# Optimization experiments

Measured on AMD Instinct MI355X. Metric: run time of the kernel, lower is better.

The kernel has to match this reference:

```python
import jax, jax.numpy as jnp
import numpy as np

B, L, ENC, D, H, HD, MLP, R = 4, 512, 512, 1024, 16, 64, 4096, 32
NUM_BUCKETS, MAX_DISTANCE = 32, 128
EPS = 1e-6
NEG = -1e10


def rmsnorm(x, scale):
    var = jnp.mean(jnp.square(x), axis=-1, keepdims=True)
    return x * jax.lax.rsqrt(var + EPS) * scale


def rel_pos_bias(table, qlen, klen):
    # T5 causal (bidirectional=False) relative position bucketing.
    ctx = jnp.arange(qlen)[:, None]
    mem = jnp.arange(klen)[None, :]
    rp = mem - ctx                      # [q, k]
    n = -jnp.minimum(rp, 0)             # distance into the past
    max_exact = NUM_BUCKETS // 2
    is_small = n < max_exact
    large = max_exact + (
        jnp.log(jnp.maximum(n, 1).astype(jnp.float32) / max_exact)
        / np.log(MAX_DISTANCE / max_exact) * (NUM_BUCKETS - max_exact)
    ).astype(jnp.int32)
    large = jnp.minimum(large, NUM_BUCKETS - 1)
    bucket = jnp.where(is_small, n, large)
    return table[bucket].transpose(2, 0, 1)[None]  # [1, h, q, k]


def lora_dense(x, W, a, b):
    # x:[B,L,d]  W:[d,e]  a:[B,d,r]  b:[B,r,e]  -> xW + (xa)b per example
    out = jnp.einsum('bld,de->ble', x, W)
    low = jnp.einsum('bld,bdr->blr', x, a)
    return out + jnp.einsum('blr,bre->ble', low, b)


def attention(xq, xkv, Wq, Wk, Wv, Wo, qa, qb, ka, kb, va, vb, oa, ob, bias):
    b, ql, _ = xq.shape
    kl = xkv.shape[1]
    q = lora_dense(xq, Wq, qa, qb).reshape(b, ql, H, HD) * (1.0 / np.sqrt(HD))
    k = lora_dense(xkv, Wk, ka, kb).reshape(b, kl, H, HD)
    v = lora_dense(xkv, Wv, va, vb).reshape(b, kl, H, HD)
    scores = jnp.einsum('bqhd,bkhd->bhqk', q, k)
    if bias is not None:
        scores = scores + bias
    probs = jax.nn.softmax(scores, axis=-1)
    ctx = jnp.einsum('bhqk,bkhd->bqhd', probs, v).reshape(b, ql, H * HD)
    return lora_dense(ctx, Wo, oa, ob)


def setup_inputs() -> dict:
    key = jax.random.key(0)
    ks = jax.random.split(key, 32)
    s = 0.02
    inp = {
        'inputs':  jax.random.normal(ks[0], (B, L, D), jnp.float32),
        'encoded': jax.random.normal(ks[1], (B, ENC, D), jnp.float32),
        'lora_qa': jax.random.normal(ks[2], (B, 2, D, R), jnp.float32) * s,
        'lora_qb': jax.random.normal(ks[3], (B, 2, R, D), jnp.float32) * s,
        'lora_ka': jax.random.normal(ks[4], (B, 2, D, R), jnp.float32) * s,
        'lora_kb': jax.random.normal(ks[5], (B, 2, R, D), jnp.float32) * s,
        'lora_va': jax.random.normal(ks[6], (B, 2, D, R), jnp.float32) * s,
        'lora_vb': jax.random.normal(ks[7], (B, 2, R, D), jnp.float32) * s,
        'lora_oa': jax.random.normal(ks[8], (B, 2, D, R), jnp.float32) * s,
        'lora_ob': jax.random.normal(ks[9], (B, 2, R, D), jnp.float32) * s,
        'rel_table': jax.random.normal(ks[10], (NUM_BUCKETS, H), jnp.float32) * s,
        'ln1': jnp.ones((D,), jnp.float32),
        'ln2': jnp.ones((D,), jnp.float32),
        'ln3': jnp.ones((D,), jnp.float32),
        'sWq': jax.random.normal(ks[11], (D, H * HD), jnp.float32) * s,
        'sWk': jax.random.normal(ks[12], (D, H * HD), jnp.float32) * s,
        'sWv': jax.random.normal(ks[13], (D, H * HD), jnp.float32) * s,
        'sWo': jax.random.normal(ks[14], (H * HD, D), jnp.float32) * s,
        'cWq': jax.random.normal(ks[15], (D, H * HD), jnp.float32) * s,
        'cWk': jax.random.normal(ks[16], (D, H * HD), jnp.float32) * s,
        'cWv': jax.random.normal(ks[17], (D, H * HD), jnp.float32) * s,
        'cWo': jax.random.normal(ks[18], (H * HD, D), jnp.float32) * s,
        'wi0': jax.random.normal(ks[19], (D, MLP), jnp.float32) * s,
        'wi1': jax.random.normal(ks[20], (D, MLP), jnp.float32) * s,
        'wo_mlp': jax.random.normal(ks[21], (MLP, D), jnp.float32) * s,
    }
    return inp


def reference(inputs, encoded, lora_qa, lora_qb, lora_ka, lora_kb, lora_va, lora_vb,
              lora_oa, lora_ob, rel_table, ln1, ln2, ln3,
              sWq, sWk, sWv, sWo, cWq, cWk, cWv, cWo, wi0, wi1, wo_mlp):
    l = inputs.shape[1]
    causal = jnp.tril(jnp.ones((l, l), dtype=bool))
    dec_bias = rel_pos_bias(rel_table, l, l) + jnp.where(causal, 0.0, NEG)[None, None]

    # --- self-attention block ---
    x = rmsnorm(inputs, ln1)
    x = attention(x, x, sWq, sWk, sWv, sWo,
                  lora_qa[:, 0], lora_qb[:, 0], lora_ka[:, 0], lora_kb[:, 0],
                  lora_va[:, 0], lora_vb[:, 0], lora_oa[:, 0], lora_ob[:, 0],
                  dec_bias)
    x = x + inputs

    # --- cross-attention block ---
    y = rmsnorm(x, ln2)
    y = attention(y, encoded, cWq, cWk, cWv, cWo,
                  lora_qa[:, 1], lora_qb[:, 1], lora_ka[:, 1], lora_kb[:, 1],
                  lora_va[:, 1], lora_vb[:, 1], lora_oa[:, 1], lora_ob[:, 1],
                  None)
    y = y + x

    # --- gated-gelu MLP block (T5 v1.1 style) ---
    lz = rmsnorm(y, ln3)
    h = jax.nn.gelu(lz @ wi0, approximate=False) * (lz @ wi1)
    z = h @ wo_mlp + y
    return z
```

## Files before the change

kernel.cpp:

```cpp
#include <hip/hip_runtime.h>
#include <math.h>


#define DEV __device__ __forceinline__

typedef __bf16 bf16x8 __attribute__((ext_vector_type(8)));
typedef float floatx4 __attribute__((ext_vector_type(4)));

typedef __attribute__((address_space(1))) void* gas_ptr;
typedef __attribute__((address_space(3))) void* las_ptr;

DEV unsigned short f2bf(float f) {
  union { float f; unsigned int u; } v; v.f = f;
  unsigned int r = v.u + 0x7fffu + ((v.u >> 16) & 1u);
  return (unsigned short)(r >> 16);
}
DEV float bf2f(unsigned short u) {
  union { unsigned int u; float f; } v; v.u = ((unsigned int)u) << 16;
  return v.f;
}

#define GLOAD_LDS16(g, l) __builtin_amdgcn_global_load_lds((gas_ptr)(g), (las_ptr)(l), 16, 0, 0)

template<int NW>
DEV void stage_tile_sw(const char* gbase, char* lds, int nrows, int ldbytes, int wave, int lane) {
  int nchunks = nrows >> 3;
  int colb = (((lane & 7) ^ ((lane >> 3) & 7)) << 4);
  for (int c = wave; c < nchunks; c += NW) {
    int row = (c << 3) + (lane >> 3);
    GLOAD_LDS16(gbase + (size_t)row * ldbytes + colb, lds + (c << 10));
  }
}

template<int NW>
DEV void stage_tile256_sw(const char* gbase, char* lds, int nrows, int ldbytes, int wave, int lane) {
  int nchunks = nrows >> 2;
  for (int c = wave; c < nchunks; c += NW) {
    int row = (c << 2) + (lane >> 4);
    int key = row & 7;
    int colb = ((lane & 15) ^ key) << 4;
    GLOAD_LDS16(gbase + (size_t)row * ldbytes + colb, lds + (c << 10));
  }
}

template<int WM, int WN>
DEV void gemm_core(const unsigned short* A, const unsigned short* Bt, float* C,
                   int K, int lda, int ldb, int ldc, int m0, int n0,
                   char* ldsA, char* ldsB) {
  constexpr int NW = WM * WN;
  const int tid  = threadIdx.x;
  const int lane = tid & 63;
  const int wave = tid >> 6;
  const int wm   = wave % WM;
  const int wn   = wave / WM;
  const int quad = lane >> 4;
  const int l15  = lane & 15;
  const int key  = l15 & 7;

  floatx4 acc[4][4];
#pragma unroll
  for (int i = 0; i < 4; ++i)
#pragma unroll
    for (int j = 0; j < 4; ++j) acc[i][j] = (floatx4){0.f, 0.f, 0.f, 0.f};

  const char* gA = (const char*)(A + (size_t)m0 * lda);
  const char* gB = (const char*)(Bt + (size_t)n0 * ldb);

  for (int k0 = 0; k0 < K; k0 += 64) {
    stage_tile_sw<NW>(gA + (size_t)k0 * 2, ldsA, WM * 64, lda * 2, wave, lane);
    stage_tile_sw<NW>(gB + (size_t)k0 * 2, ldsB, WN * 64, ldb * 2, wave, lane);
    __syncthreads();
#pragma unroll
    for (int kk = 0; kk < 64; kk += 32) {
      bf16x8 af[4], bv[4];
      int off = (((kk >> 3) + quad) ^ key) << 4;
      const char* baseA = ldsA + (size_t)(wm * 64 + l15) * 128 + off;
      const char* baseB = ldsB + (size_t)(wn * 64 + l15) * 128 + off;
#pragma unroll
      for (int mi = 0; mi < 4; ++mi) af[mi] = *(const bf16x8*)(baseA + mi * 2048);
#pragma unroll
      for (int ni = 0; ni < 4; ++ni) bv[ni] = *(const bf16x8*)(baseB + ni * 2048);
#pragma unroll
      for (int mi = 0; mi < 4; ++mi)
#pragma unroll
        for (int ni = 0; ni < 4; ++ni)
          acc[mi][ni] = __builtin_amdgcn_mfma_f32_16x16x32_bf16(af[mi], bv[ni], acc[mi][ni], 0, 0, 0);
    }
    __syncthreads();
  }

#pragma unroll
  for (int mi = 0; mi < 4; ++mi) {
#pragma unroll
    for (int r = 0; r < 4; ++r) {
      int row = m0 + wm * 64 + mi * 16 + quad * 4 + r;
#pragma unroll
      for (int ni = 0; ni < 4; ++ni) {
        int col = n0 + wn * 64 + ni * 16 + l15;
        C[(size_t)row * ldc + col] = acc[mi][ni][r];
      }
    }
  }
}

__global__ __launch_bounds__(256) void k_gemm1s(const unsigned short* A, const unsigned short* Bt,
                                                float* Cpart, size_t pstride,
                                                int Kchunk, int lda, int ldb, int ldc) {
  __shared__ char lds[32768];
  int s = blockIdx.z;
  size_t koff = (size_t)s * Kchunk;
  gemm_core<2, 2>(A + koff, Bt + koff, Cpart + (size_t)s * pstride,
                  Kchunk, lda, ldb, ldc,
                  blockIdx.y * 128, blockIdx.x * 128, lds, lds + 16384);
}

struct GXSlice {
  const unsigned short* A0;
  const unsigned short* Aext;
  const unsigned short* B0;
  const unsigned short* Bext;
  float* C;
  size_t bextb;
  int ldc, nxa, it0, it1;
};
struct GX { GXSlice s[4]; };

__global__ __launch_bounds__(256) void k_gemmx(GX g) {
  __shared__ char lds[32768];
  char* ldsA = lds;
  char* ldsB = lds + 16384;
  GXSlice sl = g.s[blockIdx.z];
  if ((int)blockIdx.x >= sl.nxa) return;
  const int m0 = blockIdx.y * 128, n0 = blockIdx.x * 128;
  const int b = m0 >> 9;
  const int tid = threadIdx.x, lane = tid & 63, wave = tid >> 6;
  const int wm = wave & 1, wn = wave >> 1;
  const int quad = lane >> 4, l15 = lane & 15;
  const int key = l15 & 7;

  floatx4 acc[4][4];
#pragma unroll
  for (int i = 0; i < 4; ++i)
#pragma unroll
    for (int j = 0; j < 4; ++j) acc[i][j] = (floatx4){0.f, 0.f, 0.f, 0.f};

  for (int it = sl.it0; it < sl.it1; ++it) {
    if (it < 16) {
      stage_tile_sw<4>((const char*)sl.A0 + (size_t)m0 * 2048 + it * 128, ldsA, 128, 2048, wave, lane);
      stage_tile_sw<4>((const char*)sl.B0 + (size_t)n0 * 2048 + it * 128, ldsB, 128, 2048, wave, lane);
    } else {
      int eb = (it - 16) * 128;
      stage_tile_sw<4>((const char*)sl.Aext + (size_t)m0 * 256 + eb, ldsA, 128, 256, wave, lane);
      stage_tile_sw<4>((const char*)(sl.Bext + (size_t)b * sl.bextb) + (size_t)n0 * 256 + eb,
                       ldsB, 128, 256, wave, lane);
    }
    __syncthreads();
#pragma unroll
    for (int kk = 0; kk < 64; kk += 32) {
      bf16x8 af[4], bv[4];
      int off = (((kk >> 3) + quad) ^ key) << 4;
      const char* baseA = ldsA + (size_t)(wm * 64 + l15) * 128 + off;
      const char* baseB = ldsB + (size_t)(wn * 64 + l15) * 128 + off;
#pragma unroll
      for (int mi = 0; mi < 4; ++mi) af[mi] = *(const bf16x8*)(baseA + mi * 2048);
#pragma unroll
      for (int ni = 0; ni < 4; ++ni) bv[ni] = *(const bf16x8*)(baseB + ni * 2048);
#pragma unroll
      for (int mi = 0; mi < 4; ++mi)
#pragma unroll
        for (int ni = 0; ni < 4; ++ni)
          acc[mi][ni] = __builtin_amdgcn_mfma_f32_16x16x32_bf16(af[mi], bv[ni], acc[mi][ni], 0, 0, 0);
    }
    __syncthreads();
  }

#pragma unroll
  for (int mi = 0; mi < 4; ++mi) {
#pragma unroll
    for (int r = 0; r < 4; ++r) {
      int row = m0 + wm * 64 + mi * 16 + quad * 4 + r;
#pragma unroll
      for (int ni = 0; ni < 4; ++ni) {
        int col = n0 + wn * 64 + ni * 16 + l15;
        sl.C[(size_t)row * sl.ldc + col] = acc[mi][ni][r];
      }
    }
  }
}

__global__ __launch_bounds__(256) void k_qkvsum(const float* bqs, const float* bqc,
                                                unsigned short* qbf, unsigned short* kbf,
                                                unsigned short* kbf2) {
  const size_t PS = (size_t)2048 * 3072, PC = (size_t)2048 * 2048;
  int t = threadIdx.x;
  int row0 = blockIdx.x * 8;
  int zc = blockIdx.y;
  for (int j = 0; j < 8; ++j) {
    int row = row0 + j;
    int nsec = zc ? 1 : 2;
    for (int sec = 0; sec < nsec; ++sec) {
      const float* base = zc ? (bqc + (size_t)row * 2048 + sec * 1024)
                             : (bqs + (size_t)row * 3072 + sec * 1024);
      float4 a = ((const float4*)base)[t];
      float4 c = ((const float4*)(base + (zc ? PC : PS)))[t];
      float4 s; s.x = a.x + c.x; s.y = a.y + c.y; s.z = a.z + c.z; s.w = a.w + c.w;
      ushort4 o; o.x = f2bf(s.x); o.y = f2bf(s.y); o.z = f2bf(s.z); o.w = f2bf(s.w);
      unsigned short* dst = zc ? kbf2 : (sec == 0 ? qbf : kbf);
      ((ushort4*)(dst + (size_t)row * 1024))[t] = o;
    }
  }
}

__global__ __launch_bounds__(256) void k_vtrans2(const float* bqs, const float* bqc,
                                                 unsigned short* vtb, unsigned short* vtb2) {
  __shared__ float tl[64][65];
  int which = blockIdx.z;
  int z = blockIdx.y, b = z >> 4, h = z & 15;
  int k0 = blockIdx.x * 64;
  int ld = which ? 2048 : 3072;
  int voff = which ? 1024 : 2048;
  const float* src = which ? bqc : bqs;
  size_t PARTW = (size_t)2048 * ld;
  unsigned short* dst = which ? vtb2 : vtb;
  int t = threadIdx.x;
  {
    int kr = t >> 2, c0 = (t & 3) * 16;
    const float* p = src + (size_t)(b * 512 + k0 + kr) * ld + voff + h * 64 + c0;
    float4 v0[4], v1[4];
#pragma unroll
    for (int i = 0; i < 4; ++i) {
      v0[i] = *(const float4*)(p + i * 4);
      v1[i] = *(const float4*)(p + PARTW + i * 4);
    }
#pragma unroll
    for (int i = 0; i < 4; ++i) {
      tl[kr][c0 + i * 4 + 0] = v0[i].x + v1[i].x;
      tl[kr][c0 + i * 4 + 1] = v0[i].y + v1[i].y;
      tl[kr][c0 + i * 4 + 2] = v0[i].z + v1[i].z;
      tl[kr][c0 + i * 4 + 3] = v0[i].w + v1[i].w;
    }
  }
  __syncthreads();
  {
    int dw = t >> 2, kc = (t & 3) * 16;
    union { unsigned short us[16]; uint4 q[2]; } pk;
#pragma unroll
    for (int j = 0; j < 16; ++j) pk.us[j] = f2bf(tl[kc + j][dw]);
    uint4* dp = (uint4*)(dst + ((size_t)z * 64 + dw) * 512 + k0 + kc);
    dp[0] = pk.q[0]; dp[1] = pk.q[1];
  }
}

template<bool CAUSAL, bool QSUM>
__global__ __launch_bounds__(256) void k_flash(const unsigned short* qmat, const float* qparts,
                                               const unsigned short* kmat, const unsigned short* vt,
                                               const float* rb, unsigned short* ctxb) {
  __shared__ char ldsQ[8192];
  __shared__ char ldsK[16384];
  __shared__ char ldsV[16384];
  __shared__ char ldsP[16384];
  __shared__ float lrb[512];

  const size_t PART = (size_t)2048 * 1024;
  const int z = blockIdx.y, b = z >> 4, h = z & 15;
  const int q0 = blockIdx.x * 64;
  const int tid = threadIdx.x, lane = tid & 63, wave = tid >> 6;
  const int quad = lane >> 4, l15 = lane & 15;
  const int key = l15 & 7;

  const unsigned short* K = kmat + (size_t)b * 512 * 1024 + h * 64;
  const unsigned short* V = vt + (size_t)z * 64 * 512;

  if (QSUM) {
#pragma unroll
    for (int rr = 0; rr < 4; ++rr) {
      int row = rr * 16 + (tid >> 4);
      int c4 = tid & 15;
      const float* src = qparts + (size_t)(q0 + row) * 1024 + h * 64 + c4 * 4;
      float4 s0 = *(const float4*)src;
      float4 s1 = *(const float4*)(src + PART);
      float4 s2 = *(const float4*)(src + 2 * PART);
      float4 s3 = *(const float4*)(src + 3 * PART);
      ushort4 o;
      o.x = f2bf(s0.x + s1.x + s2.x + s3.x);
      o.y = f2bf(s0.y + s1.y + s2.y + s3.y);
      o.z = f2bf(s0.z + s1.z + s2.z + s3.z);
      o.w = f2bf(s0.w + s1.w + s2.w + s3.w);
      int qoff = (((c4 >> 1) ^ (row & 7)) << 4) | ((c4 & 1) << 3);
      *(ushort4*)(ldsQ + (size_t)row * 128 + qoff) = o;
    }
  } else {
    const unsigned short* Q = qmat + (size_t)b * 512 * 1024 + h * 64;
    stage_tile_sw<4>((const char*)(Q + (size_t)q0 * 1024), ldsQ, 64, 2048, wave, lane);
  }
  if (CAUSAL)
    for (int i = tid; i < 512; i += 256) lrb[i] = rb[h * 512 + i];

  float m_run[4], l_run[4];
  floatx4 oacc[4];
#pragma unroll
  for (int r = 0; r < 4; ++r) { m_run[r] = -1e30f; l_run[r] = 0.f; }
#pragma unroll
  for (int ni = 0; ni < 4; ++ni) oacc[ni] = (floatx4){0.f, 0.f, 0.f, 0.f};

  const int ktend = CAUSAL ? (blockIdx.x / 2 + 1) : 4;
  for (int kt = 0; kt < ktend; ++kt) {
    __syncthreads();
    stage_tile_sw<4>((const char*)(K + (size_t)kt * 128 * 1024), ldsK, 128, 2048, wave, lane);
    stage_tile256_sw<4>((const char*)(V + kt * 128), ldsV, 64, 1024, wave, lane);
    __syncthreads();

    floatx4 sacc[8];
#pragma unroll
    for (int ct = 0; ct < 8; ++ct) sacc[ct] = (floatx4){0.f, 0.f, 0.f, 0.f};
    const size_t qrow = (size_t)(wave * 16 + l15) * 128;
#pragma unroll
    for (int kd = 0; kd < 2; ++kd) {
      int offq = ((quad + kd * 4) ^ key) << 4;
      bf16x8 af = *(const bf16x8*)(ldsQ + qrow + offq);
#pragma unroll
      for (int ct = 0; ct < 8; ++ct) {
        bf16x8 bfv = *(const bf16x8*)(ldsK + (size_t)(ct * 16 + l15) * 128 + offq);
        sacc[ct] = __builtin_amdgcn_mfma_f32_16x16x32_bf16(af, bfv, sacc[ct], 0, 0, 0);
      }
    }

    float sv[8][4];
#pragma unroll
    for (int ct = 0; ct < 8; ++ct)
#pragma unroll
      for (int r = 0; r < 4; ++r) {
        float v = sacc[ct][r] * 0.125f;
        if (CAUSAL) {
          int qq = q0 + wave * 16 + quad * 4 + r;
          int kk = kt * 128 + ct * 16 + l15;
          v = (kk <= qq) ? v + lrb[qq - kk] : -1e30f;
        }
        sv[ct][r] = v;
      }

    float mx[4];
#pragma unroll
    for (int r = 0; r < 4; ++r) {
      mx[r] = sv[0][r];
#pragma unroll
      for (int ct = 1; ct < 8; ++ct) mx[r] = fmaxf(mx[r], sv[ct][r]);
    }
#pragma unroll
    for (int o = 1; o < 16; o <<= 1)
#pragma unroll
      for (int r = 0; r < 4; ++r) mx[r] = fmaxf(mx[r], __shfl_xor(mx[r], o));

    float alpha[4], rs[4];
#pragma unroll
    for (int r = 0; r < 4; ++r) {
      float mn = fmaxf(m_run[r], mx[r]);
      alpha[r] = __expf(m_run[r] - mn);
      m_run[r] = mn;
      rs[r] = 0.f;
    }
#pragma unroll
    for (int ct = 0; ct < 8; ++ct)
#pragma unroll
      for (int r = 0; r < 4; ++r) {
        float p = __expf(sv[ct][r] - m_run[r]);
        sv[ct][r] = p;
        rs[r] += p;
      }
#pragma unroll
    for (int o = 1; o < 16; o <<= 1)
#pragma unroll
      for (int r = 0; r < 4; ++r) rs[r] += __shfl_xor(rs[r], o);
#pragma unroll
    for (int r = 0; r < 4; ++r) l_run[r] = l_run[r] * alpha[r] + rs[r];
#pragma unroll
    for (int ni = 0; ni < 4; ++ni)
#pragma unroll
      for (int r = 0; r < 4; ++r) oacc[ni][r] *= alpha[r];

#pragma unroll
    for (int ct = 0; ct < 8; ++ct)
#pragma unroll
      for (int r = 0; r < 4; ++r) {
        int prow_w = wave * 16 + quad * 4 + r;
        int kidx = ct * 16 + l15;
        int pb = (((kidx >> 3) ^ (prow_w & 7)) << 4) | ((kidx & 7) << 1);
        *(unsigned short*)(ldsP + (size_t)prow_w * 256 + pb) = f2bf(sv[ct][r]);
      }
    __syncthreads();

    const size_t prow = (size_t)(wave * 16 + l15) * 256;
#pragma unroll
    for (int kk = 0; kk < 4; ++kk) {
      int offp = ((quad + kk * 4) ^ key) << 4;
      bf16x8 pf = *(const bf16x8*)(ldsP + prow + offp);
#pragma unroll
      for (int ni = 0; ni < 4; ++ni) {
        bf16x8 vf8 = *(const bf16x8*)(ldsV + (size_t)(ni * 16 + l15) * 256 + offp);
        oacc[ni] = __builtin_amdgcn_mfma_f32_16x16x32_bf16(pf, vf8, oacc[ni], 0, 0, 0);
      }
    }
  }

#pragma unroll
  for (int r = 0; r < 4; ++r) {
    int q = q0 + wave * 16 + quad * 4 + r;
    float inv = 1.0f / l_run[r];
    unsigned short* dst = ctxb + ((size_t)b * 512 + q) * 1024 + h * 64;
#pragma unroll
    for (int ni = 0; ni < 4; ++ni)
      dst[ni * 16 + l15] = f2bf(oacc[ni][r] * inv);
  }
}

__global__ __launch_bounds__(512) void k_mlp(const unsigned short* A, const unsigned short* Wc,
                                             unsigned short* hbf) {
  __shared__ char lds[49152];
  char* ldsA = lds;
  char* ldsB = lds + 16384;
  const int m0 = blockIdx.y * 128;
  const int n0 = blockIdx.x * 128;
  const int tid = threadIdx.x, lane = tid & 63, wave = tid >> 6;
  const int half = wave >> 2, wl = wave & 3;
  const int wm = wl & 1, wn = wl >> 1;
  const int quad = lane >> 4, l15 = lane & 15;
  const int key = l15 & 7;

  floatx4 acc[4][4];
#pragma unroll
  for (int i = 0; i < 4; ++i)
#pragma unroll
    for (int j = 0; j < 4; ++j) acc[i][j] = (floatx4){0.f, 0.f, 0.f, 0.f};

  const char* gA = (const char*)(A + (size_t)m0 * 1024);
  const char* gB = (const char*)(Wc + (size_t)blockIdx.x * 256 * 1024);

  for (int k0 = 0; k0 < 1024; k0 += 64) {
    stage_tile_sw<8>(gA + (size_t)k0 * 2, ldsA, 128, 2048, wave, lane);
    stage_tile_sw<8>(gB + (size_t)k0 * 2, ldsB, 256, 2048, wave, lane);
    __syncthreads();
#pragma unroll
    for (int kk = 0; kk < 64; kk += 32) {
      bf16x8 af[4], bv[4];
      int off = (((kk >> 3) + quad) ^ key) << 4;
      const char* baseA = ldsA + (size_t)(wm * 64 + l15) * 128 + off;
      const char* baseB = ldsB + (size_t)(half * 128 + wn * 64 + l15) * 128 + off;
#pragma unroll
      for (int mi = 0; mi < 4; ++mi) af[mi] = *(const bf16x8*)(baseA + mi * 2048);
#pragma unroll
      for (int ni = 0; ni < 4; ++ni) bv[ni] = *(const bf16x8*)(baseB + ni * 2048);
#pragma unroll
      for (int mi = 0; mi < 4; ++mi)
#pragma unroll
        for (int ni = 0; ni < 4; ++ni)
          acc[mi][ni] = __builtin_amdgcn_mfma_f32_16x16x32_bf16(af[mi], bv[ni], acc[mi][ni], 0, 0, 0);
    }
    __syncthreads();
  }

  if (half == 1) {
#pragma unroll
    for (int mi = 0; mi < 4; ++mi)
#pragma unroll
      for (int r = 0; r < 4; ++r) {
        int row = wm * 64 + mi * 16 + quad * 4 + r;
#pragma unroll
        for (int ni = 0; ni < 4; ++ni) {
          int col = wn * 64 + ni * 16 + l15;
          *(unsigned short*)(ldsB + (size_t)row * 256 + col * 2) = f2bf(acc[mi][ni][r]);
        }
      }
  }
  __syncthreads();
  if (half == 0) {
#pragma unroll
    for (int mi = 0; mi < 4; ++mi)
#pragma unroll
      for (int r = 0; r < 4; ++r) {
        int row = wm * 64 + mi * 16 + quad * 4 + r;
#pragma unroll
        for (int ni = 0; ni < 4; ++ni) {
          int col = wn * 64 + ni * 16 + l15;
          float h1 = bf2f(*(const unsigned short*)(ldsB + (size_t)row * 256 + col * 2));
          float g = acc[mi][ni][r];
          float v = 0.5f * g * (1.0f + erff(g * 0.70710678f)) * h1;
          hbf[(size_t)(m0 + row) * 4096 + n0 + col] = f2bf(v);
        }
      }
  }
}

struct PrepArgs {
  const float* src[11];
  unsigned short* dst[11];
  int K[11], N[11], mode[11];
  int tstart[12];
  const float* encoded;
  unsigned short* encbf;
  const float* table;
  float* rb;
  unsigned short* bmdst[5];
  const float* bmsrc[5][3];
  int bmnrg[5];
  int bmstart[6];
  int nwt, nf2bf, nbm;
};
__global__ __launch_bounds__(256, 2) void k_prep(PrepArgs a) {
  __shared__ float tl[64][65];
  int bid = blockIdx.x;
  int t = threadIdx.x;
  if (bid < a.nwt) {
    int z = 0;
    while (z < 10 && bid >= a.tstart[z + 1]) ++z;
    int tile = bid - a.tstart[z];
    int N = a.N[z], K = a.K[z], mode = a.mode[z];
    int ntn = N >> 6;
    int tn = tile % ntn, tk = tile / ntn;
    const float* src = a.src[z] + (size_t)(tk * 64) * N + tn * 64;
    unsigned short* dst = a.dst[z];
    {
      int rq = t >> 4, c4 = (t & 15) * 4;
      float4 v[4];
#pragma unroll
      for (int i = 0; i < 4; ++i)
        v[i] = *(const float4*)(src + (size_t)(rq + i * 16) * N + c4);
#pragma unroll
      for (int i = 0; i < 4; ++i) {
        int r = rq + i * 16;
        tl[r][c4] = v[i].x; tl[r][c4 + 1] = v[i].y;
        tl[r][c4 + 2] = v[i].z; tl[r][c4 + 3] = v[i].w;
      }
    }
    __syncthreads();
    {
      int nl = t >> 2, kseg = (t & 3) * 16;
      int n = tn * 64 + nl;
      int orow = (mode == 0) ? n : ((n >> 7) * 256 + ((mode == 2) ? 128 : 0) + (n & 127));
      union { unsigned short us[16]; uint4 q[2]; } pk;
#pragma unroll
      for (int j = 0; j < 16; ++j) pk.us[j] = f2bf(tl[kseg + j][nl]);
      uint4* dp = (uint4*)(dst + (size_t)orow * K + tk * 64 + kseg);
      dp[0] = pk.q[0]; dp[1] = pk.q[1];
    }
    return;
  }
  bid -= a.nwt;
  if (bid < a.nf2bf) {
    const float4* src = (const float4*)a.encoded;
    ushort4* dst = (ushort4*)a.encbf;
    int base = bid * 2048 + t;
    float4 v[8];
#pragma unroll
    for (int i = 0; i < 8; ++i) v[i] = src[base + i * 256];
#pragma unroll
    for (int i = 0; i < 8; ++i) {
      ushort4 o;
      o.x = f2bf(v[i].x); o.y = f2bf(v[i].y); o.z = f2bf(v[i].z); o.w = f2bf(v[i].w);
      dst[base + i * 256] = o;
    }
    return;
  }
  bid -= a.nf2bf;
  if (bid < 32) {
    int i = bid * 256 + t;
    if (i < 16 * 512) {
      int h = i >> 9, d = i & 511;
      int bucket;
      if (d < 16) bucket = d;
      else {
        int lb = 16 + (int)(logf((float)d / 16.0f) / logf(8.0f) * 16.0f);
        bucket = lb < 31 ? lb : 31;
      }
      a.rb[i] = a.table[bucket * 16 + h];
    }
    return;
  }
  bid -= 32;
  {
    int m = 0;
    while (m < 4 && bid >= a.bmstart[m + 1]) ++m;
    int idx = bid - a.bmstart[m];
    int nrg = a.bmnrg[m];
    int b = idx / nrg, rg = idx % nrg;
    int n0 = rg * 128;
    int sec = n0 >> 10;
    const float* src = a.bmsrc[m][sec] + (size_t)b * 65536;
    unsigned short* dst = a.bmdst[m] + ((size_t)b * nrg * 128 + n0) * 128;
    int n = t & 127, coff = (t >> 7) * 64;
    int ncol = (n0 & 1023) + n;
    unsigned short* drow = dst + (size_t)n * 128 + coff;
    for (int cg = 0; cg < 16; cg += 8) {
      float vv[8][4];
#pragma unroll
      for (int cc = 0; cc < 8; ++cc)
#pragma unroll
        for (int e = 0; e < 4; ++e) {
          int c = coff + (cg + cc) * 4 + e;
          vv[cc][e] = ((c >> 5) == sec) ? src[(size_t)(c & 31) * 1024 + ncol] : 0.f;
        }
#pragma unroll
      for (int cc = 0; cc < 8; ++cc) {
        ushort4 o;
        o.x = f2bf(vv[cc][0]); o.y = f2bf(vv[cc][1]);
        o.z = f2bf(vv[cc][2]); o.w = f2bf(vv[cc][3]);
        *(ushort4*)(drow + (cg + cc) * 4) = o;
      }
    }
  }
}

__global__ __launch_bounds__(256) void k_lowc(const float* encoded, const float* a0g,
                                              const float* a1g, unsigned short* lowc) {
  __shared__ float rowsF[8 * 1024];
  __shared__ float pacc[2 * 8 * 8 * 32];
  int t = threadIdx.x;
  int row0 = blockIdx.x * 8;
  int b = row0 >> 9;
  for (int j = 0; j < 8; ++j)
    ((float4*)(rowsF + j * 1024))[t] = ((const float4*)(encoded + (size_t)(row0 + j) * 1024))[t];
  __syncthreads();
  int r = t & 31, g = t >> 5;
  float acc[2][8];
#pragma unroll
  for (int p = 0; p < 2; ++p)
#pragma unroll
    for (int j = 0; j < 8; ++j) acc[p][j] = 0.f;
  const float* a0 = a0g + (size_t)b * 65536;
  const float* a1 = a1g + (size_t)b * 65536;
  for (int i = 0; i < 128; ++i) {
    int k = g * 128 + i;
    float ak = a0[(size_t)k * 32 + r];
    float av = a1[(size_t)k * 32 + r];
#pragma unroll
    for (int j = 0; j < 8; ++j) {
      float x = rowsF[j * 1024 + k];
      acc[0][j] += x * ak;
      acc[1][j] += x * av;
    }
  }
#pragma unroll
  for (int p = 0; p < 2; ++p)
#pragma unroll
    for (int j = 0; j < 8; ++j)
      pacc[((p * 8 + j) * 8 + g) * 32 + r] = acc[p][j];
  __syncthreads();
  for (int j = 0; j < 8; ++j) {
    if (t < 64) {
      int p = t >> 5, r2 = t & 31;
      float s = 0.f;
      for (int gg = 0; gg < 8; ++gg) s += pacc[((p * 8 + j) * 8 + gg) * 32 + r2];
      lowc[(size_t)(row0 + j) * 128 + p * 32 + r2] = f2bf(s);
    } else if (t < 128) {
      lowc[(size_t)(row0 + j) * 128 + t] = 0;
    }
  }
}

__global__ __launch_bounds__(256) void k_start(const float* x, const float* sc,
                                               const float* qa, const float* ka, const float* va,
                                               unsigned short* xn, unsigned short* lowext) {
  __shared__ unsigned short lrows[8][1024];
  __shared__ float pacc[3 * 8 * 8 * 32];
  __shared__ float red[4];
  int t = threadIdx.x;
  int row0 = blockIdx.x * 8;
  int b = row0 >> 9;
  float4 s4 = ((const float4*)sc)[t];
  for (int j = 0; j < 8; ++j) {
    int row = row0 + j;
    float4 v = ((const float4*)(x + (size_t)row * 1024))[t];
    float ss = v.x * v.x + v.y * v.y + v.z * v.z + v.w * v.w;
    for (int o = 32; o; o >>= 1) ss += __shfl_down(ss, o);
    if ((t & 63) == 0) red[t >> 6] = ss;
    __syncthreads();
    float tot = red[0] + red[1] + red[2] + red[3];
    float rs = rsqrtf(tot * (1.0f / 1024.0f) + 1e-6f);
    ushort4 o;
    o.x = f2bf(v.x * rs * s4.x); o.y = f2bf(v.y * rs * s4.y);
    o.z = f2bf(v.z * rs * s4.z); o.w = f2bf(v.w * rs * s4.w);
    ((ushort4*)(xn + (size_t)row * 1024))[t] = o;
    *(ushort4*)(&lrows[j][t * 4]) = o;
    __syncthreads();
  }
  int r = t & 31, g = t >> 5;
  float acc[3][8];
#pragma unroll
  for (int p = 0; p < 3; ++p)
#pragma unroll
    for (int j = 0; j < 8; ++j) acc[p][j] = 0.f;
  const float* aq = qa + (size_t)b * 65536;
  const float* ak = ka + (size_t)b * 65536;
  const float* av = va + (size_t)b * 65536;
  for (int i = 0; i < 128; ++i) {
    int k = g * 128 + i;
    float a0 = aq[(size_t)k * 32 + r];
    float a1 = ak[(size_t)k * 32 + r];
    float a2 = av[(size_t)k * 32 + r];
#pragma unroll
    for (int j = 0; j < 8; ++j) {
      float xv = bf2f(lrows[j][k]);
      acc[0][j] += xv * a0;
      acc[1][j] += xv * a1;
      acc[2][j] += xv * a2;
    }
  }
#pragma unroll
  for (int p = 0; p < 3; ++p)
#pragma unroll
    for (int j = 0; j < 8; ++j)
      pacc[((p * 8 + j) * 8 + g) * 32 + r] = acc[p][j];
  __syncthreads();
  for (int j = 0; j < 8; ++j) {
    if (t < 96) {
      int p = t >> 5, r2 = t & 31;
      float s = 0.f;
      for (int gg = 0; gg < 8; ++gg) s += pacc[((p * 8 + j) * 8 + gg) * 32 + r2];
      lowext[(size_t)(row0 + j) * 128 + p * 32 + r2] = f2bf(s);
    } else if (t < 128) {
      lowext[(size_t)(row0 + j) * 128 + t] = 0;
    }
  }
}

template<bool LOW>
__global__ __launch_bounds__(256) void k_addbrms(const float* parts, const float* resid,
                                                 const float* sc, float* resout,
                                                 unsigned short* xn,
                                                 const float* aP, unsigned short* lowext) {
  __shared__ unsigned short lrows[8][1024];
  __shared__ float pacc[8 * 8 * 32];
  __shared__ float red[4];
  const size_t PART = (size_t)2048 * 1024;
  int t = threadIdx.x;
  int row0 = blockIdx.x * 8;
  int b = row0 >> 9;
  float4 s4 = ((const float4*)sc)[t];
  for (int j = 0; j < 8; ++j) {
    int row = row0 + j;
    const float* p0 = parts + (size_t)row * 1024;
    float4 v = ((const float4*)p0)[t];
    float4 v1 = ((const float4*)(p0 + PART))[t];
    float4 v2 = ((const float4*)(p0 + 2 * PART))[t];
    float4 v3 = ((const float4*)(p0 + 3 * PART))[t];
    float4 rv = ((const float4*)(resid + (size_t)row * 1024))[t];
    float4 s;
    s.x = v.x + v1.x + v2.x + v3.x + rv.x;
    s.y = v.y + v1.y + v2.y + v3.y + rv.y;
    s.z = v.z + v1.z + v2.z + v3.z + rv.z;
    s.w = v.w + v1.w + v2.w + v3.w + rv.w;
    ((float4*)(resout + (size_t)row * 1024))[t] = s;
    float ss = s.x * s.x + s.y * s.y + s.z * s.z + s.w * s.w;
    for (int o = 32; o; o >>= 1) ss += __shfl_down(ss, o);
    if ((t & 63) == 0) red[t >> 6] = ss;
    __syncthreads();
    float tot = red[0] + red[1] + red[2] + red[3];
    float rs = rsqrtf(tot * (1.0f / 1024.0f) + 1e-6f);
    ushort4 o;
    o.x = f2bf(s.x * rs * s4.x); o.y = f2bf(s.y * rs * s4.y);
    o.z = f2bf(s.z * rs * s4.z); o.w = f2bf(s.w * rs * s4.w);
    ((ushort4*)(xn + (size_t)row * 1024))[t] = o;
    if (LOW) *(ushort4*)(&lrows[j][t * 4]) = o;
    __syncthreads();
  }
  if (LOW) {
    int r = t & 31, g = t >> 5;
    float acc[8];
#pragma unroll
    for (int j = 0; j < 8; ++j) acc[j] = 0.f;
    const float* ap = aP + (size_t)b * 65536;
    for (int i = 0; i < 128; ++i) {
      int k = g * 128 + i;
      float a0 = ap[(size_t)k * 32 + r];
#pragma unroll
      for (int j = 0; j < 8; ++j) acc[j] += bf2f(lrows[j][k]) * a0;
    }
#pragma unroll
    for (int j = 0; j < 8; ++j) pacc[(j * 8 + g) * 32 + r] = acc[j];
    __syncthreads();
    for (int j = 0; j < 8; ++j) {
      if (t < 32) {
        float s = 0.f;
        for (int gg = 0; gg < 8; ++gg) s += pacc[(j * 8 + gg) * 32 + t];
        lowext[(size_t)(row0 + j) * 128 + t] = f2bf(s);
      } else if (t < 128) {
        lowext[(size_t)(row0 + j) * 128 + t] = 0;
      }
    }
  }
}

__global__ __launch_bounds__(256) void k_lowbf(const unsigned short* x, const float* a,
                                               unsigned short* lowext) {
  int row0 = blockIdx.x * 8;
  int b = row0 >> 9;
  int t = threadIdx.x, r = t & 31, j = t >> 5;
  int row = row0 + j;
  const bf16x8* xv = (const bf16x8*)(x + (size_t)row * 1024);
  const float* ap = a + (size_t)b * 65536;
  float s = 0.f;
  for (int kb = 0; kb < 128; ++kb) {
    bf16x8 v = xv[kb];
#pragma unroll
    for (int u = 0; u < 8; ++u)
      s += (float)v[u] * ap[(size_t)(kb * 8 + u) * 32 + r];
  }
  lowext[(size_t)row * 128 + r] = f2bf(s);
  lowext[(size_t)row * 128 + 32 + r] = 0;
  lowext[(size_t)row * 128 + 64 + r] = 0;
  lowext[(size_t)row * 128 + 96 + r] = 0;
}

__global__ void k_sum4(const float* p, size_t pstride, const float* resid, float* out) {
  int i = blockIdx.x * 256 + threadIdx.x;
  float4 a = ((const float4*)p)[i];
  float4 b = ((const float4*)(p + pstride))[i];
  float4 c = ((const float4*)(p + 2 * pstride))[i];
  float4 d = ((const float4*)(p + 3 * pstride))[i];
  float4 r = ((const float4*)resid)[i];
  float4 o;
  o.x = a.x + b.x + c.x + d.x + r.x;
  o.y = a.y + b.y + c.y + d.y + r.y;
  o.z = a.z + b.z + c.z + d.z + r.z;
  o.w = a.w + b.w + c.w + d.w + r.w;
  ((float4*)out)[i] = o;
}


extern "C" void kernel_launch(void* const* d_in, const int* in_sizes, int n_in,
                              void* d_out, int out_size, void* d_ws, size_t ws_size,
                              hipStream_t stream) {
  const float* f_inputs  = (const float*)d_in[0];
  const float* f_encoded = (const float*)d_in[1];
  const float* f_qa = (const float*)d_in[2];
  const float* f_qb = (const float*)d_in[3];
  const float* f_ka = (const float*)d_in[4];
  const float* f_kb = (const float*)d_in[5];
  const float* f_va = (const float*)d_in[6];
  const float* f_vb = (const float*)d_in[7];
  const float* f_oa = (const float*)d_in[8];
  const float* f_ob = (const float*)d_in[9];
  const float* f_table = (const float*)d_in[10];
  const float* f_ln1 = (const float*)d_in[11];
  const float* f_ln2 = (const float*)d_in[12];
  const float* f_ln3 = (const float*)d_in[13];
  const float* f_W[8] = { (const float*)d_in[14], (const float*)d_in[15],
                          (const float*)d_in[16], (const float*)d_in[17],
                          (const float*)d_in[18], (const float*)d_in[19],
                          (const float*)d_in[20], (const float*)d_in[21] };
  const float* f_wi0 = (const float*)d_in[22];
  const float* f_wi1 = (const float*)d_in[23];
  const float* f_wo  = (const float*)d_in[24];

  const size_t SEL1 = 32768;
  const size_t PART = (size_t)2048 * 1024;

  char* w = (char*)d_ws;
  size_t off = 0;
  auto alloc = [&](size_t bytes) -> char* {
    off = (off + 255) & ~(size_t)255;
    char* p = w + off;
    off += bytes;
    return p;
  };
  unsigned short* wt  = (unsigned short*)alloc((size_t)8192 * 1024 * 2);
  unsigned short* wc  = (unsigned short*)alloc((size_t)8192 * 1024 * 2);
  unsigned short* wot = (unsigned short*)alloc((size_t)1024 * 4096 * 2);
  unsigned short* encbf = (unsigned short*)alloc(2048 * 1024 * 2);
  float* rb = (float*)alloc(16 * 512 * 4);
  unsigned short* xn  = (unsigned short*)alloc(2048 * 1024 * 2);
  unsigned short* qbf = (unsigned short*)alloc(2048 * 1024 * 2);
  unsigned short* kbf = (unsigned short*)alloc(2048 * 1024 * 2);
  unsigned short* vtb = (unsigned short*)alloc((size_t)64 * 64 * 512 * 2);
  unsigned short* kbf2 = (unsigned short*)alloc(2048 * 1024 * 2);
  unsigned short* vtb2 = (unsigned short*)alloc((size_t)64 * 64 * 512 * 2);
  unsigned short* lowext_s = (unsigned short*)alloc(2048 * 128 * 2);
  unsigned short* lowext_c = (unsigned short*)alloc(2048 * 128 * 2);
  unsigned short* lowext_q = (unsigned short*)alloc(2048 * 128 * 2);
  unsigned short* lowext_o = (unsigned short*)alloc(2048 * 128 * 2);
  unsigned short* bmext_s  = (unsigned short*)alloc((size_t)4 * 3072 * 128 * 2);
  unsigned short* bmext_c  = (unsigned short*)alloc((size_t)4 * 2048 * 128 * 2);
  unsigned short* bmext_q  = (unsigned short*)alloc((size_t)4 * 1024 * 128 * 2);
  unsigned short* bmext_o  = (unsigned short*)alloc((size_t)4 * 1024 * 128 * 2);
  unsigned short* bmext_o2 = (unsigned short*)alloc((size_t)4 * 1024 * 128 * 2);
  unsigned short* ctxb = (unsigned short*)alloc(2048 * 1024 * 2);
  float* xres = (float*)alloc(2048 * 1024 * 4);
  float* yres = (float*)alloc(2048 * 1024 * 4);
  char*  big  = alloc((size_t)84 << 20);
  float* bqs  = (float*)big;
  float* bqc  = (float*)(big + ((size_t)48 << 20));
  float* op_s = (float*)big;
  float* qp_c = (float*)(big + ((size_t)32 << 20));
  float* op_c = (float*)big;
  unsigned short* hbf = (unsigned short*)big;
  float* fp   = (float*)(big + ((size_t)16 << 20));
  (void)ws_size; (void)in_sizes; (void)n_in; (void)out_size;

  PrepArgs pa;
  int ts = 0;
  for (int i = 0; i < 8; ++i) {
    pa.src[i] = f_W[i]; pa.dst[i] = wt + (size_t)i * 1024 * 1024;
    pa.K[i] = 1024; pa.N[i] = 1024; pa.mode[i] = 0;
    pa.tstart[i] = ts; ts += 256;
  }
  pa.src[8] = f_wi0; pa.dst[8] = wc; pa.K[8] = 1024; pa.N[8] = 4096; pa.mode[8] = 1;
  pa.tstart[8] = ts; ts += 1024;
  pa.src[9] = f_wi1; pa.dst[9] = wc; pa.K[9] = 1024; pa.N[9] = 4096; pa.mode[9] = 2;
  pa.tstart[9] = ts; ts += 1024;
  pa.src[10] = f_wo; pa.dst[10] = wot; pa.K[10] = 4096; pa.N[10] = 1024; pa.mode[10] = 0;
  pa.tstart[10] = ts; ts += 1024;
  pa.tstart[11] = ts;
  pa.nwt = ts;
  pa.encoded = f_encoded; pa.encbf = encbf;
  pa.table = f_table; pa.rb = rb;
  pa.nf2bf = 256;
  pa.bmdst[0] = bmext_s;  pa.bmnrg[0] = 24;
  pa.bmsrc[0][0] = f_qb; pa.bmsrc[0][1] = f_kb; pa.bmsrc[0][2] = f_vb;
  pa.bmdst[1] = bmext_c;  pa.bmnrg[1] = 16;
  pa.bmsrc[1][0] = f_kb + SEL1; pa.bmsrc[1][1] = f_vb + SEL1; pa.bmsrc[1][2] = nullptr;
  pa.bmdst[2] = bmext_q;  pa.bmnrg[2] = 8;
  pa.bmsrc[2][0] = f_qb + SEL1; pa.bmsrc[2][1] = nullptr; pa.bmsrc[2][2] = nullptr;
  pa.bmdst[3] = bmext_o;  pa.bmnrg[3] = 8;
  pa.bmsrc[3][0] = f_ob; pa.bmsrc[3][1] = nullptr; pa.bmsrc[3][2] = nullptr;
  pa.bmdst[4] = bmext_o2; pa.bmnrg[4] = 8;
  pa.bmsrc[4][0] = f_ob + SEL1; pa.bmsrc[4][1] = nullptr; pa.bmsrc[4][2] = nullptr;
  int bs = 0;
  for (int m = 0; m < 5; ++m) { pa.bmstart[m] = bs; bs += pa.bmnrg[m] * 4; }
  pa.bmstart[5] = bs;
  pa.nbm = bs;
  int totblk = pa.nwt + pa.nf2bf + 32 + pa.nbm;
  k_prep<<<dim3(totblk), dim3(256), 0, stream>>>(pa);
  k_lowc<<<dim3(256), dim3(256), 0, stream>>>(f_encoded, f_ka + SEL1, f_va + SEL1, lowext_c);

  k_start<<<dim3(256), dim3(256), 0, stream>>>(f_inputs, f_ln1, f_qa, f_ka, f_va, xn, lowext_s);

  {
    GX g;
    const size_t PS = (size_t)2048 * 3072, PC = (size_t)2048 * 2048;
    g.s[0] = { xn, lowext_s, wt, bmext_s, bqs,            (size_t)3072 * 128, 3072, 24, 0, 9 };
    g.s[1] = { xn, lowext_s, wt, bmext_s, bqs + PS,       (size_t)3072 * 128, 3072, 24, 9, 18 };
    g.s[2] = { encbf, lowext_c, wt + (size_t)5120 * 1024, bmext_c, bqc,      (size_t)2048 * 128, 2048, 16, 0, 9 };
    g.s[3] = { encbf, lowext_c, wt + (size_t)5120 * 1024, bmext_c, bqc + PC, (size_t)2048 * 128, 2048, 16, 9, 18 };
    k_gemmx<<<dim3(24, 16, 4), dim3(256), 0, stream>>>(g);
  }
  k_qkvsum<<<dim3(256, 2), dim3(256), 0, stream>>>(bqs, bqc, qbf, kbf, kbf2);
  k_vtrans2<<<dim3(8, 64, 2), dim3(256), 0, stream>>>(bqs, bqc, vtb, vtb2);

  k_flash<true, false><<<dim3(8, 64), dim3(256), 0, stream>>>(qbf, nullptr, kbf, vtb, rb, ctxb);

  k_lowbf<<<dim3(256), dim3(256), 0, stream>>>(ctxb, f_oa, lowext_o);
  {
    GX g;
    for (int s = 0; s < 4; ++s)
      g.s[s] = { ctxb, lowext_o, wt + (size_t)3072 * 1024, bmext_o, op_s + (size_t)s * PART,
                 (size_t)1024 * 128, 1024, 8, s * 18 / 4, (s + 1) * 18 / 4 };
    k_gemmx<<<dim3(8, 16, 4), dim3(256), 0, stream>>>(g);
  }
  k_addbrms<true><<<dim3(256), dim3(256), 0, stream>>>(op_s, f_inputs, f_ln2, xres, xn,
                                                       f_qa + SEL1, lowext_q);

  {
    GX g;
    for (int s = 0; s < 4; ++s)
      g.s[s] = { xn, lowext_q, wt + (size_t)4096 * 1024, bmext_q, qp_c + (size_t)s * PART,
                 (size_t)1024 * 128, 1024, 8, s * 18 / 4, (s + 1) * 18 / 4 };
    k_gemmx<<<dim3(8, 16, 4), dim3(256), 0, stream>>>(g);
  }
  k_flash<false, true><<<dim3(8, 64), dim3(256), 0, stream>>>(nullptr, qp_c, kbf2, vtb2, rb, ctxb);

  k_lowbf<<<dim3(256), dim3(256), 0, stream>>>(ctxb, f_oa + SEL1, lowext_o);
  {
    GX g;
    for (int s = 0; s < 4; ++s)
      g.s[s] = { ctxb, lowext_o, wt + (size_t)7168 * 1024, bmext_o2, op_c + (size_t)s * PART,
                 (size_t)1024 * 128, 1024, 8, s * 18 / 4, (s + 1) * 18 / 4 };
    k_gemmx<<<dim3(8, 16, 4), dim3(256), 0, stream>>>(g);
  }
  k_addbrms<false><<<dim3(256), dim3(256), 0, stream>>>(op_c, xres, f_ln3, yres, xn,
                                                        nullptr, nullptr);

  k_mlp<<<dim3(32, 16), dim3(512), 0, stream>>>(xn, wc, hbf);
  k_gemm1s<<<dim3(8, 16, 4), dim3(256), 0, stream>>>(hbf, wot, fp, PART, 1024, 4096, 4096, 1024);
  k_sum4<<<dim3(2048), dim3(256), 0, stream>>>(fp, PART, yres, (float*)d_out);
}
```

Measured before the change: 579.1 us.

## Fuse QKV projection GEMM with bf16 conversion and V transpose epilogue

Replaces the split-K QKV GEMM, which wrote fp32 partials, and the separate sum/convert and V-transpose kernels with one GEMM. That GEMM runs the full K loop per tile and writes bf16 Q/K directly, plus V transposed through LDS in the epilogue. This removes large fp32 intermediate writes and reads and two kernel launches. In exchange the grid halves from 4 to 2 split slices, so each block runs a longer K loop and parallelism drops.

```diff
diff --git a/kernel.cpp b/kernel.cpp
--- a/kernel.cpp
+++ b/kernel.cpp
@@ -188,66 +188,113 @@
   }
 }
 
-__global__ __launch_bounds__(256) void k_qkvsum(const float* bqs, const float* bqc,
-                                                unsigned short* qbf, unsigned short* kbf,
-                                                unsigned short* kbf2) {
-  const size_t PS = (size_t)2048 * 3072, PC = (size_t)2048 * 2048;
-  int t = threadIdx.x;
-  int row0 = blockIdx.x * 8;
-  int zc = blockIdx.y;
-  for (int j = 0; j < 8; ++j) {
-    int row = row0 + j;
-    int nsec = zc ? 1 : 2;
-    for (int sec = 0; sec < nsec; ++sec) {
-      const float* base = zc ? (bqc + (size_t)row * 2048 + sec * 1024)
-                             : (bqs + (size_t)row * 3072 + sec * 1024);
-      float4 a = ((const float4*)base)[t];
-      float4 c = ((const float4*)(base + (zc ? PC : PS)))[t];
-      float4 s; s.x = a.x + c.x; s.y = a.y + c.y; s.z = a.z + c.z; s.w = a.w + c.w;
-      ushort4 o; o.x = f2bf(s.x); o.y = f2bf(s.y); o.z = f2bf(s.z); o.w = f2bf(s.w);
-      unsigned short* dst = zc ? kbf2 : (sec == 0 ? qbf : kbf);
-      ((ushort4*)(dst + (size_t)row * 1024))[t] = o;
-    }
-  }
-}
-
-__global__ __launch_bounds__(256) void k_vtrans2(const float* bqs, const float* bqc,
-                                                 unsigned short* vtb, unsigned short* vtb2) {
-  __shared__ float tl[64][65];
-  int which = blockIdx.z;
-  int z = blockIdx.y, b = z >> 4, h = z & 15;
-  int k0 = blockIdx.x * 64;
-  int ld = which ? 2048 : 3072;
-  int voff = which ? 1024 : 2048;
-  const float* src = which ? bqc : bqs;
-  size_t PARTW = (size_t)2048 * ld;
-  unsigned short* dst = which ? vtb2 : vtb;
-  int t = threadIdx.x;
-  {
-    int kr = t >> 2, c0 = (t & 3) * 16;
-    const float* p = src + (size_t)(b * 512 + k0 + kr) * ld + voff + h * 64 + c0;
-    float4 v0[4], v1[4];
-#pragma unroll
-    for (int i = 0; i < 4; ++i) {
-      v0[i] = *(const float4*)(p + i * 4);
-      v1[i] = *(const float4*)(p + PARTW + i * 4);
-    }
-#pragma unroll
-    for (int i = 0; i < 4; ++i) {
-      tl[kr][c0 + i * 4 + 0] = v0[i].x + v1[i].x;
-      tl[kr][c0 + i * 4 + 1] = v0[i].y + v1[i].y;
-      tl[kr][c0 + i * 4 + 2] = v0[i].z + v1[i].z;
-      tl[kr][c0 + i * 4 + 3] = v0[i].w + v1[i].w;
-    }
-  }
-  __syncthreads();
-  {
-    int dw = t >> 2, kc = (t & 3) * 16;
-    union { unsigned short us[16]; uint4 q[2]; } pk;
-#pragma unroll
-    for (int j = 0; j < 16; ++j) pk.us[j] = f2bf(tl[kc + j][dw]);
-    uint4* dp = (uint4*)(dst + ((size_t)z * 64 + dw) * 512 + k0 + kc);
-    dp[0] = pk.q[0]; dp[1] = pk.q[1];
+struct QKVSlice {
+  const unsigned short* A0;
+  const unsigned short* Aext;
+  const unsigned short* B0;
+  const unsigned short* Bext;
+  unsigned short* sec0;
+  unsigned short* sec1;
+  unsigned short* sec2;
+  size_t bextb;
+  int vsec, nxa;
+};
+struct QKV2 { QKVSlice s[2]; };
+
+__global__ __launch_bounds__(256) void k_gemmqkv(QKV2 g) {
+  __shared__ char lds[34816];
+  char* ldsA = lds;
+  char* ldsB = lds + 16384;
+  QKVSlice sl = g.s[blockIdx.z];
+  if ((int)blockIdx.x >= sl.nxa) return;
+  const int m0 = blockIdx.y * 128, n0 = blockIdx.x * 128;
+  const int b = m0 >> 9;
+  const int tid = threadIdx.x, lane = tid & 63, wave = tid >> 6;
+  const int wm = wave & 1, wn = wave >> 1;
+  const int quad = lane >> 4, l15 = lane & 15;
+  const int key = l15 & 7;
+
+  floatx4 acc[4][4];
+#pragma unroll
+  for (int i = 0; i < 4; ++i)
+#pragma unroll
+    for (int j = 0; j < 4; ++j) acc[i][j] = (floatx4){0.f, 0.f, 0.f, 0.f};
+
+  for (int it = 0; it < 18; ++it) {
+    if (it < 16) {
+      stage_tile_sw<4>((const char*)sl.A0 + (size_t)m0 * 2048 + it * 128, ldsA, 128, 2048, wave, lane);
+      stage_tile_sw<4>((const char*)sl.B0 + (size_t)n0 * 2048 + it * 128, ldsB, 128, 2048, wave, lane);
+    } else {
+      int eb = (it - 16) * 128;
+      stage_tile_sw<4>((const char*)sl.Aext + (size_t)m0 * 256 + eb, ldsA, 128, 256, wave, lane);
+      stage_tile_sw<4>((const char*)(sl.Bext + (size_t)b * sl.bextb) + (size_t)n0 * 256 + eb,
+                       ldsB, 128, 256, wave, lane);
+    }
+    __syncthreads();
+#pragma unroll
+    for (int kk = 0; kk < 64; kk += 32) {
+      bf16x8 af[4], bv[4];
+      int off = (((kk >> 3) + quad) ^ key) << 4;
+      const char* baseA = ldsA + (size_t)(wm * 64 + l15) * 128 + off;
+      const char* baseB = ldsB + (size_t)(wn * 64 + l15) * 128 + off;
+#pragma unroll
+      for (int mi = 0; mi < 4; ++mi) af[mi] = *(const bf16x8*)(baseA + mi * 2048);
+#pragma unroll
+      for (int ni = 0; ni < 4; ++ni) bv[ni] = *(const bf16x8*)(baseB + ni * 2048);
+#pragma unroll
+      for (int mi = 0; mi < 4; ++mi)
+#pragma unroll
+        for (int ni = 0; ni < 4; ++ni)
+          acc[mi][ni] = __builtin_amdgcn_mfma_f32_16x16x32_bf16(af[mi], bv[ni], acc[mi][ni], 0, 0, 0);
+    }
+    __syncthreads();
+  }
+
+  const int sec = n0 >> 10;
+  const int nloc = n0 & 1023;
+  if (sec != sl.vsec) {
+    unsigned short* dst = (sec == 0) ? sl.sec0 : sl.sec1;
+#pragma unroll
+    for (int mi = 0; mi < 4; ++mi)
+#pragma unroll
+      for (int r = 0; r < 4; ++r) {
+        int row = m0 + wm * 64 + mi * 16 + quad * 4 + r;
+        unsigned short* drow = dst + (size_t)row * 1024 + nloc + wn * 64;
+#pragma unroll
+        for (int ni = 0; ni < 4; ++ni)
+          drow[ni * 16 + l15] = f2bf(acc[mi][ni][r]);
+      }
+  } else {
+    unsigned short* vdstb = (sl.vsec == 1) ? sl.sec1 : sl.sec2;
+    char* vbuf = lds + (size_t)(wm * 2 + wn) * 8704;
+#pragma unroll
+    for (int ni = 0; ni < 4; ++ni)
+#pragma unroll
+      for (int mi = 0; mi < 4; ++mi) {
+        unsigned long long pk =
+            (unsigned long long)f2bf(acc[mi][ni][0])
+          | ((unsigned long long)f2bf(acc[mi][ni][1]) << 16)
+          | ((unsigned long long)f2bf(acc[mi][ni][2]) << 32)
+          | ((unsigned long long)f2bf(acc[mi][ni][3]) << 48);
+        *(unsigned long long*)(vbuf + (size_t)(ni * 16 + l15) * 136 + (mi * 16 + quad * 4) * 2) = pk;
+      }
+    __syncthreads();
+    int dbase = nloc + wn * 64;
+    int h = dbase >> 6;
+    int kb = (m0 & 511) + wm * 64;
+    unsigned short* vdst = vdstb + (size_t)(b * 16 + h) * 64 * 512;
+    int lh = lane >> 3, ll = lane & 7;
+#pragma unroll
+    for (int i = 0; i < 8; ++i) {
+      int d = i * 8 + lh;
+      const char* p = vbuf + (size_t)d * 136 + ll * 16;
+      unsigned long long lo = *(const unsigned long long*)p;
+      unsigned long long hi = *(const unsigned long long*)(p + 8);
+      uint4 v;
+      v.x = (unsigned)lo; v.y = (unsigned)(lo >> 32);
+      v.z = (unsigned)hi; v.w = (unsigned)(hi >> 32);
+      *(uint4*)(vdst + (size_t)d * 512 + kb + ll * 8) = v;
+    }
   }
 }
 
@@ -886,8 +933,6 @@
   float* xres = (float*)alloc(2048 * 1024 * 4);
   float* yres = (float*)alloc(2048 * 1024 * 4);
   char*  big  = alloc((size_t)84 << 20);
-  float* bqs  = (float*)big;
-  float* bqc  = (float*)(big + ((size_t)48 << 20));
   float* op_s = (float*)big;
   float* qp_c = (float*)(big + ((size_t)32 << 20));
   float* op_c = (float*)big;
@@ -934,16 +979,13 @@
   k_start<<<dim3(256), dim3(256), 0, stream>>>(f_inputs, f_ln1, f_qa, f_ka, f_va, xn, lowext_s);
 
   {
-    GX g;
-    const size_t PS = (size_t)2048 * 3072, PC = (size_t)2048 * 2048;
-    g.s[0] = { xn, lowext_s, wt, bmext_s, bqs,            (size_t)3072 * 128, 3072, 24, 0, 9 };
-    g.s[1] = { xn, lowext_s, wt, bmext_s, bqs + PS,       (size_t)3072 * 128, 3072, 24, 9, 18 };
-    g.s[2] = { encbf, lowext_c, wt + (size_t)5120 * 1024, bmext_c, bqc,      (size_t)2048 * 128, 2048, 16, 0, 9 };
-    g.s[3] = { encbf, lowext_c, wt + (size_t)5120 * 1024, bmext_c, bqc + PC, (size_t)2048 * 128, 2048, 16, 9, 18 };
-    k_gemmx<<<dim3(24, 16, 4), dim3(256), 0, stream>>>(g);
-  }
-  k_qkvsum<<<dim3(256, 2), dim3(256), 0, stream>>>(bqs, bqc, qbf, kbf, kbf2);
-  k_vtrans2<<<dim3(8, 64, 2), dim3(256), 0, stream>>>(bqs, bqc, vtb, vtb2);
+    QKV2 g;
+    g.s[0] = { xn, lowext_s, wt, bmext_s,
+               qbf, kbf, vtb, (size_t)3072 * 128, 2, 24 };
+    g.s[1] = { encbf, lowext_c, wt + (size_t)5120 * 1024, bmext_c,
+               kbf2, vtb2, nullptr, (size_t)2048 * 128, 1, 16 };
+    k_gemmqkv<<<dim3(24, 16, 2), dim3(256), 0, stream>>>(g);
+  }
 
   k_flash<true, false><<<dim3(8, 64), dim3(256), 0, stream>>>(qbf, nullptr, kbf, vtb, rb, ctxb);
 
```

Result: faster. 549.5 us (-5.1%).
